# Optimization experiments

Hardware: AMD Instinct MI355X
Metric: run time of the kernel (lower is better)

The kernel has to match this reference:

```python
import jax, jax.numpy as jnp
import numpy as np

HIDDEN = 512
HEADS = 8
NORM = 1.0 / np.sqrt(HIDDEN // HEADS)  # torch: 1/sqrt(tensor(dim_k)//head) = 1/8


def setup_inputs() -> dict:
    key = jax.random.key(0)
    ks = jax.random.split(key, 14)
    B, N, D = 2, 2048, HIDDEN
    s = 0.02
    d = {
        "x_re": jax.random.normal(ks[0], (B, N, D), dtype=jnp.float32),
        "x_im": jax.random.normal(ks[1], (B, N, D), dtype=jnp.float32),
    }
    names = ["Wq_re", "Wq_im", "bq_re", "bq_im",
             "Wk_re", "Wk_im", "bk_re", "bk_im",
             "Wv_re", "Wv_im", "bv_re", "bv_im"]
    for i, nm in enumerate(names):
        shape = (D, D) if nm.startswith("W") else (D,)
        d[nm] = jax.random.normal(ks[2 + i], shape, dtype=jnp.float32) * s
    return d


def reference(x_re, x_im,
              Wq_re, Wq_im, bq_re, bq_im,
              Wk_re, Wk_im, bk_re, bk_im,
              Wv_re, Wv_im, bv_re, bv_im):
    B, N, D = x_re.shape
    h, dk = HEADS, D // HEADS
    x = jax.lax.complex(x_re, x_im)
    Wq = jax.lax.complex(Wq_re, Wq_im); bq = jax.lax.complex(bq_re, bq_im)
    Wk = jax.lax.complex(Wk_re, Wk_im); bk = jax.lax.complex(bk_re, bk_im)
    Wv = jax.lax.complex(Wv_re, Wv_im); bv = jax.lax.complex(bv_re, bv_im)

    def proj(W, b):  # torch nn.Linear: x @ W.T + b, then split heads -> [B,h,N,dk]
        y = x @ W.T + b
        return y.reshape(B, N, h, dk).transpose(0, 2, 1, 3)

    q, k, v = proj(Wq, bq), proj(Wk, bk), proj(Wv, bv)
    # complex matmul (no conjugation, matching torch.matmul), scaled
    dist = jnp.einsum("bhnd,bhmd->bhnm", q, k) * NORM
    probs = jax.nn.softmax(jnp.abs(dist), axis=-1).astype(jnp.complex64)
    att = jnp.einsum("bhnm,bhmd->bhnd", probs, v)
    att = att.transpose(0, 2, 1, 3).reshape(B, N, D)
    # real-view output [B, N, D, 2]
    return jnp.stack([att.real, att.imag], axis=-1)
```

## Files before the change

kernel.cpp:

```cpp
#include <hip/hip_runtime.h>
#include <hip/hip_bf16.h>
#include <math.h>

#define B_ 2
#define N_ 2048
#define D_ 512
#define H_ 8
#define DK_ 64
#define M_ (B_ * N_)

typedef short s16x8 __attribute__((ext_vector_type(8)));
typedef short s16x4 __attribute__((ext_vector_type(4)));
typedef float fx4   __attribute__((ext_vector_type(4)));
typedef int   ix4   __attribute__((ext_vector_type(4)));

static __device__ __forceinline__ short f2bf(float f) {
    __hip_bfloat16 h = __float2bfloat16(f);
    return __builtin_bit_cast(short, h);
}
static __device__ __forceinline__ float bf2f(short s) {
    unsigned int u = ((unsigned int)(unsigned short)s) << 16;
    return __builtin_bit_cast(float, u);
}
static __device__ __forceinline__ float fexp2(float x) {
#if __has_builtin(__builtin_amdgcn_exp2f)
    return __builtin_amdgcn_exp2f(x);
#else
    return exp2f(x);
#endif
}
static __device__ __forceinline__ float fsqrt_(float x) {
#if __has_builtin(__builtin_amdgcn_sqrtf)
    return __builtin_amdgcn_sqrtf(x);
#else
    return sqrtf(x);
#endif
}
static __device__ __forceinline__ int pack_tr(float a, float b) {
    unsigned ua = __builtin_bit_cast(unsigned, a);
    unsigned ub = __builtin_bit_cast(unsigned, b);
    return (int)((ua >> 16) | (ub & 0xFFFF0000u));
}

#define MFMA16(a, b, c) __builtin_amdgcn_mfma_f32_16x16x32_bf16(a, b, c, 0, 0, 0)

#define C2_ 0.18033688f
#define M0_ 16.0f

__global__ __launch_bounds__(256, 2)
void qkproj_mfma(const float* __restrict__ xr, const float* __restrict__ xi,
                 const float* __restrict__ W0r, const float* __restrict__ W0i,
                 const float* __restrict__ b0r, const float* __restrict__ b0i,
                 const float* __restrict__ W1r, const float* __restrict__ W1i,
                 const float* __restrict__ b1r, const float* __restrict__ b1i,
                 short* __restrict__ o0r, short* __restrict__ o0i,
                 short* __restrict__ o1r, short* __restrict__ o1i)
{
    __shared__ short sA[2][128][40];
    __shared__ short sB[2][64][40];

    const int tid = threadIdx.x;
    const int w = tid >> 6, l = tid & 63, lg = l >> 4, lc = l & 15;
    const int wr = w >> 1, wc = w & 1;
    const int bn = blockIdx.x, bm = blockIdx.y, z = blockIdx.z;
    const float* Wr = z ? W1r : W0r;
    const float* Wi = z ? W1i : W0i;
    const float* br = z ? b1r : b0r;
    const float* bi = z ? b1i : b0i;
    short* outr = z ? o1r : o0r;
    short* outi = z ? o1i : o0i;

    const int srow = tid >> 3, scol = (tid & 7) * 4;
    int aoff = (bm * 128 + srow) * D_ + scol;
    int boff = (bn * 64 + srow) * D_ + scol;

    float4 rA[8], rB[4];
    auto issue = [&]() {
#pragma unroll
        for (int u = 0; u < 8; ++u) {
            const float* src = (u >= 4) ? xi : xr;
            rA[u] = *(const float4*)&src[aoff + (u & 3) * 32 * D_];
        }
#pragma unroll
        for (int u = 0; u < 4; ++u) {
            const float* src = (u >= 2) ? Wi : Wr;
            rB[u] = *(const float4*)&src[boff + (u & 1) * 32 * D_];
        }
        aoff += 32; boff += 32;
    };

    fx4 Cre[4][2], Cim[4][2];
#pragma unroll
    for (int mf = 0; mf < 4; ++mf)
#pragma unroll
        for (int nf = 0; nf < 2; ++nf)
#pragma unroll
            for (int j = 0; j < 4; ++j) { Cre[mf][nf][j] = 0.f; Cim[mf][nf][j] = 0.f; }

    issue();
    for (int k0 = 0; k0 < D_; k0 += 32) {
        __syncthreads();
#pragma unroll
        for (int u = 0; u < 8; ++u) {
            int comp = u >> 2, row = (u & 3) * 32 + srow;
            float vv[4] = {rA[u].x, rA[u].y, rA[u].z, rA[u].w};
            s16x4 hv;
#pragma unroll
            for (int q = 0; q < 4; ++q) hv[q] = f2bf(vv[q]);
            *(s16x4*)&sA[comp][row][scol] = hv;
        }
#pragma unroll
        for (int u = 0; u < 4; ++u) {
            int comp = u >> 1, row = (u & 1) * 32 + srow;
            float vv[4] = {rB[u].x, rB[u].y, rB[u].z, rB[u].w};
            s16x4 hv;
#pragma unroll
            for (int q = 0; q < 4; ++q) hv[q] = f2bf(vv[q]);
            *(s16x4*)&sB[comp][row][scol] = hv;
        }
        __syncthreads();
        if (k0 + 32 < D_) issue();

        s16x8 a[2][4];
#pragma unroll
        for (int comp = 0; comp < 2; ++comp)
#pragma unroll
            for (int mf = 0; mf < 4; ++mf)
                a[comp][mf] = *(const s16x8*)&sA[comp][wr * 64 + mf * 16 + lc][lg * 8];
        s16x8 bfr[2][2], bin[2];
#pragma unroll
        for (int comp = 0; comp < 2; ++comp)
#pragma unroll
            for (int nf = 0; nf < 2; ++nf)
                bfr[comp][nf] = *(const s16x8*)&sB[comp][wc * 32 + nf * 16 + lc][lg * 8];
#pragma unroll
        for (int nf = 0; nf < 2; ++nf) bin[nf] = bfr[1][nf] ^ (short)0x8000;

        __builtin_amdgcn_s_setprio(1);
#pragma unroll
        for (int mf = 0; mf < 4; ++mf)
#pragma unroll
            for (int nf = 0; nf < 2; ++nf) {
                Cre[mf][nf] = MFMA16(a[0][mf], bfr[0][nf], Cre[mf][nf]);
                Cre[mf][nf] = MFMA16(a[1][mf], bin[nf],    Cre[mf][nf]);
                Cim[mf][nf] = MFMA16(a[0][mf], bfr[1][nf], Cim[mf][nf]);
                Cim[mf][nf] = MFMA16(a[1][mf], bfr[0][nf], Cim[mf][nf]);
            }
        __builtin_amdgcn_s_setprio(0);
    }

    const int bb = (bm * 128) >> 11;
#pragma unroll
    for (int nf = 0; nf < 2; ++nf) {
        const int c = bn * 64 + wc * 32 + nf * 16 + lc;
        const float brv = br[c], biv = bi[c];
        const int h = c >> 6, dd = c & 63;
        const int n00 = (bm * 128 + wr * 64 + lg * 4) & (N_ - 1);
        size_t obase = (((size_t)(bb * H_ + h) * N_) + n00) * DK_ + dd;
#pragma unroll
        for (int mf = 0; mf < 4; ++mf)
#pragma unroll
            for (int j = 0; j < 4; ++j) {
                size_t o = obase + (size_t)(mf * 16 + j) * DK_;
                outr[o] = f2bf(Cre[mf][nf][j] + brv);
                outi[o] = f2bf(Cim[mf][nf][j] + biv);
            }
    }
}

__global__ __launch_bounds__(256, 2)
void vproj_mfma(const float* __restrict__ xr, const float* __restrict__ xi,
                const float* __restrict__ Wr, const float* __restrict__ Wi,
                const float* __restrict__ br, const float* __restrict__ bi,
                short* __restrict__ outr, short* __restrict__ outi)
{
    __shared__ short sA[2][2][64][40];
    __shared__ short sB[2][2][64][40];

    const int tid = threadIdx.x;
    const int w = tid >> 6, l = tid & 63, lg = l >> 4, lc = l & 15;
    const int wr = w >> 1, wc = w & 1;
    const int bn = blockIdx.x, bm = blockIdx.y;

    const int srow = tid >> 3, scol = (tid & 7) * 4;
    int aoff = (bm * 64 + srow) * D_ + scol;
    int boff = (bn * 64 + srow) * D_ + scol;

    float4 rA[4], rB[4];
    auto issue = [&]() {
#pragma unroll
        for (int u = 0; u < 4; ++u) {
            const float* src = (u >= 2) ? xi : xr;
            rA[u] = *(const float4*)&src[aoff + (u & 1) * 32 * D_];
        }
#pragma unroll
        for (int u = 0; u < 4; ++u) {
            const float* src = (u >= 2) ? Wi : Wr;
            rB[u] = *(const float4*)&src[boff + (u & 1) * 32 * D_];
        }
        aoff += 32; boff += 32;
    };

    fx4 Cre[2][2], Cim[2][2];
#pragma unroll
    for (int mf = 0; mf < 2; ++mf)
#pragma unroll
        for (int nf = 0; nf < 2; ++nf)
#pragma unroll
            for (int j = 0; j < 4; ++j) { Cre[mf][nf][j] = 0.f; Cim[mf][nf][j] = 0.f; }

    issue();
    for (int k0 = 0; k0 < D_; k0 += 32) {
        __syncthreads();
#pragma unroll
        for (int u = 0; u < 4; ++u) {
            int comp = u >> 1, row = (u & 1) * 32 + srow;
            float vv[4] = {rA[u].x, rA[u].y, rA[u].z, rA[u].w};
            s16x4 hv, lv;
#pragma unroll
            for (int q = 0; q < 4; ++q) {
                short hh = f2bf(vv[q]);
                hv[q] = hh;
                lv[q] = f2bf(vv[q] - bf2f(hh));
            }
            *(s16x4*)&sA[comp][0][row][scol] = hv;
            *(s16x4*)&sA[comp][1][row][scol] = lv;
        }
#pragma unroll
        for (int u = 0; u < 4; ++u) {
            int comp = u >> 1, row = (u & 1) * 32 + srow;
            float vv[4] = {rB[u].x, rB[u].y, rB[u].z, rB[u].w};
            s16x4 hv, lv;
#pragma unroll
            for (int q = 0; q < 4; ++q) {
                short hh = f2bf(vv[q]);
                hv[q] = hh;
                lv[q] = f2bf(vv[q] - bf2f(hh));
            }
            *(s16x4*)&sB[comp][0][row][scol] = hv;
            *(s16x4*)&sB[comp][1][row][scol] = lv;
        }
        __syncthreads();
        if (k0 + 32 < D_) issue();

        s16x8 a[2][2][2];
#pragma unroll
        for (int comp = 0; comp < 2; ++comp)
#pragma unroll
            for (int s = 0; s < 2; ++s)
#pragma unroll
                for (int mf = 0; mf < 2; ++mf)
                    a[comp][s][mf] = *(const s16x8*)&sA[comp][s][wr * 32 + mf * 16 + lc][lg * 8];
        s16x8 bfr[2][2][2], bin[2][2];
#pragma unroll
        for (int comp = 0; comp < 2; ++comp)
#pragma unroll
            for (int s = 0; s < 2; ++s)
#pragma unroll
                for (int nf = 0; nf < 2; ++nf)
                    bfr[comp][s][nf] = *(const s16x8*)&sB[comp][s][wc * 32 + nf * 16 + lc][lg * 8];
#pragma unroll
        for (int s = 0; s < 2; ++s)
#pragma unroll
            for (int nf = 0; nf < 2; ++nf)
                bin[s][nf] = bfr[1][s][nf] ^ (short)0x8000;

        __builtin_amdgcn_s_setprio(1);
#pragma unroll
        for (int mf = 0; mf < 2; ++mf)
#pragma unroll
            for (int nf = 0; nf < 2; ++nf) {
                fx4 cr = Cre[mf][nf], ci = Cim[mf][nf];
                cr = MFMA16(a[0][0][mf], bfr[0][0][nf], cr);
                cr = MFMA16(a[1][0][mf], bin[0][nf],    cr);
                ci = MFMA16(a[0][0][mf], bfr[1][0][nf], ci);
                ci = MFMA16(a[1][0][mf], bfr[0][0][nf], ci);
                cr = MFMA16(a[0][0][mf], bfr[0][1][nf], cr);
                cr = MFMA16(a[0][1][mf], bfr[0][0][nf], cr);
                cr = MFMA16(a[1][0][mf], bin[1][nf],    cr);
                cr = MFMA16(a[1][1][mf], bin[0][nf],    cr);
                ci = MFMA16(a[0][0][mf], bfr[1][1][nf], ci);
                ci = MFMA16(a[0][1][mf], bfr[1][0][nf], ci);
                ci = MFMA16(a[1][0][mf], bfr[0][1][nf], ci);
                ci = MFMA16(a[1][1][mf], bfr[0][0][nf], ci);
                Cre[mf][nf] = cr; Cim[mf][nf] = ci;
            }
        __builtin_amdgcn_s_setprio(0);
    }

    const int bb = (bm * 64) >> 11;
#pragma unroll
    for (int nf = 0; nf < 2; ++nf) {
        const int c = bn * 64 + wc * 32 + nf * 16 + lc;
        const float brv = br[c], biv = bi[c];
        const int h = c >> 6, dd = c & 63;
#pragma unroll
        for (int mf = 0; mf < 2; ++mf) {
            int m0 = bm * 64 + wr * 32 + mf * 16 + lg * 4;
            int n0 = m0 & (N_ - 1);
            s16x4 pr, pi;
#pragma unroll
            for (int j = 0; j < 4; ++j) {
                pr[j] = f2bf(Cre[mf][nf][j] + brv);
                pi[j] = f2bf(Cim[mf][nf][j] + biv);
            }
            size_t o = (((size_t)(bb * H_ + h) * DK_) + dd) * N_ + n0;
            *(s16x4*)&outr[o] = pr;
            *(s16x4*)&outi[o] = pi;
        }
    }
}

#define NT_ (N_ / 64)

__global__ __launch_bounds__(512, 2)
void attn_mfma(const short* __restrict__ qr, const short* __restrict__ qi,
               const short* __restrict__ kr, const short* __restrict__ ki,
               const short* __restrict__ vtr, const short* __restrict__ vti,
               float* __restrict__ out)
{
    __shared__ short sK [2][64][72];
    __shared__ short sVt[2][64][72];

    const int tid = threadIdx.x;
    const int w = tid >> 6, l = tid & 63, lg = l >> 4, lc = l & 15;
    const int qt = blockIdx.x, bh = blockIdx.y;
    const int b = bh >> 3, h = bh & 7;

    s16x8 Qr[2], Qi_[2], Qin[2];
    {
        size_t base = ((size_t)bh * N_ + (size_t)qt * 128 + w * 16 + lc) * DK_ + lg * 8;
        Qr[0]  = *(const s16x8*)&qr[base];
        Qr[1]  = *(const s16x8*)&qr[base + 32];
        Qi_[0] = *(const s16x8*)&qi[base];
        Qi_[1] = *(const s16x8*)&qi[base + 32];
        Qin[0] = Qi_[0] ^ (short)0x8000;
        Qin[1] = Qi_[1] ^ (short)0x8000;
    }

    s16x8 onesf;
#pragma unroll
    for (int u = 0; u < 8; ++u) onesf[u] = (short)0x3F80;

    fx4 o_re[4], o_im[4], o_l;
#pragma unroll
    for (int dt = 0; dt < 4; ++dt)
#pragma unroll
        for (int j = 0; j < 4; ++j) { o_re[dt][j] = 0.f; o_im[dt][j] = 0.f; }
#pragma unroll
    for (int j = 0; j < 4; ++j) o_l[j] = 0.f;

    const int rS = ((lc >> 2) << 3) | (lc & 3);

    const int srow = tid >> 3, scol8 = (tid & 7) * 8;
    int koff = bh * (N_ * DK_) + srow * DK_ + scol8;
    int voff = bh * (DK_ * N_) + srow * N_ + scol8;

    s16x8 rgK[2], rgV[2];
    auto issue = [&]() {
#pragma unroll
        for (int u = 0; u < 2; ++u) {
            const short* ksrc = u ? ki : kr;
            rgK[u] = *(const s16x8*)&ksrc[koff];
            const short* vsrc = u ? vti : vtr;
            rgV[u] = *(const s16x8*)&vsrc[voff];
        }
        koff += 64 * DK_; voff += 64;
    };

    issue();
    for (int kt = 0; kt < NT_; ++kt) {
        __syncthreads();
#pragma unroll
        for (int u = 0; u < 2; ++u) {
            *(s16x8*)&sK [u][srow][scol8] = rgK[u];
            *(s16x8*)&sVt[u][srow][scol8] = rgV[u];
        }
        __syncthreads();
        if (kt + 1 < NT_) issue();

        fx4 are[4], aim[4];
#pragma unroll
        for (int t = 0; t < 4; ++t)
#pragma unroll
            for (int j = 0; j < 4; ++j) { are[t][j] = 0.f; aim[t][j] = 0.f; }

        __builtin_amdgcn_s_setprio(1);
#pragma unroll
        for (int t = 0; t < 4; ++t) {
            const int row = rS + ((t & 1) << 2) + ((t >> 1) << 5);
#pragma unroll
            for (int c = 0; c < 2; ++c) {
                s16x8 Krf = *(const s16x8*)&sK[0][row][c * 32 + lg * 8];
                s16x8 Kif = *(const s16x8*)&sK[1][row][c * 32 + lg * 8];
                are[t] = MFMA16(Krf, Qr[c],  are[t]);
                are[t] = MFMA16(Kif, Qin[c], are[t]);
                aim[t] = MFMA16(Kif, Qr[c],  aim[t]);
                aim[t] = MFMA16(Krf, Qi_[c], aim[t]);
            }
        }
        __builtin_amdgcn_s_setprio(0);

        ix4 w0, w1;
#pragma unroll
        for (int t = 0; t < 4; ++t) {
            float p[4];
#pragma unroll
            for (int j = 0; j < 4; ++j) {
                float u2 = fmaf(are[t][j], are[t][j], aim[t][j] * aim[t][j]);
                p[j] = fexp2(fmaf(C2_, fsqrt_(u2), -M0_));
            }
            int d0 = pack_tr(p[0], p[1]);
            int d1 = pack_tr(p[2], p[3]);
            if (t == 0)      { w0[0] = d0; w0[1] = d1; }
            else if (t == 1) { w0[2] = d0; w0[3] = d1; }
            else if (t == 2) { w1[0] = d0; w1[1] = d1; }
            else             { w1[2] = d0; w1[3] = d1; }
        }
        s16x8 Pf0 = __builtin_bit_cast(s16x8, w0);
        s16x8 Pf1 = __builtin_bit_cast(s16x8, w1);

        __builtin_amdgcn_s_setprio(1);
        o_l = MFMA16(Pf0, onesf, o_l);
        o_l = MFMA16(Pf1, onesf, o_l);
#pragma unroll
        for (int dt = 0; dt < 4; ++dt) {
            s16x8 Vr0 = *(const s16x8*)&sVt[0][dt * 16 + lc][lg * 8];
            s16x8 Vi0 = *(const s16x8*)&sVt[1][dt * 16 + lc][lg * 8];
            o_re[dt] = MFMA16(Pf0, Vr0, o_re[dt]);
            o_im[dt] = MFMA16(Pf0, Vi0, o_im[dt]);
            s16x8 Vr1 = *(const s16x8*)&sVt[0][dt * 16 + lc][32 + lg * 8];
            s16x8 Vi1 = *(const s16x8*)&sVt[1][dt * 16 + lc][32 + lg * 8];
            o_re[dt] = MFMA16(Pf1, Vr1, o_re[dt]);
            o_im[dt] = MFMA16(Pf1, Vi1, o_im[dt]);
        }
        __builtin_amdgcn_s_setprio(0);
    }

    float inv[4];
#pragma unroll
    for (int j = 0; j < 4; ++j) inv[j] = 1.f / o_l[j];

    float2* po = (float2*)out;
#pragma unroll
    for (int dt = 0; dt < 4; ++dt)
#pragma unroll
        for (int j = 0; j < 4; ++j) {
            int n  = qt * 128 + w * 16 + lg * 4 + j;
            int dg = h * 64 + dt * 16 + lc;
            po[((size_t)b * N_ + n) * D_ + dg] =
                make_float2(o_re[dt][j] * inv[j], o_im[dt][j] * inv[j]);
        }
}

extern "C" void kernel_launch(void* const* d_in, const int* in_sizes, int n_in,
                              void* d_out, int out_size, void* d_ws, size_t ws_size,
                              hipStream_t stream)
{
    const float* xr = (const float*)d_in[0];
    const float* xi = (const float*)d_in[1];
    const float* Wq_r = (const float*)d_in[2];
    const float* Wq_i = (const float*)d_in[3];
    const float* bq_r = (const float*)d_in[4];
    const float* bq_i = (const float*)d_in[5];
    const float* Wk_r = (const float*)d_in[6];
    const float* Wk_i = (const float*)d_in[7];
    const float* bk_r = (const float*)d_in[8];
    const float* bk_i = (const float*)d_in[9];
    const float* Wv_r = (const float*)d_in[10];
    const float* Wv_i = (const float*)d_in[11];
    const float* bv_r = (const float*)d_in[12];
    const float* bv_i = (const float*)d_in[13];

    short* ws = (short*)d_ws;
    const size_t SZ = (size_t)B_ * H_ * N_ * DK_;
    short* qr_  = ws + 0 * SZ;
    short* qi_  = ws + 1 * SZ;
    short* kr_  = ws + 2 * SZ;
    short* ki_  = ws + 3 * SZ;
    short* vtr_ = ws + 4 * SZ;
    short* vti_ = ws + 5 * SZ;

    dim3 qkgrid(D_ / 64, M_ / 128, 2);
    qkproj_mfma<<<qkgrid, 256, 0, stream>>>(xr, xi,
                                            Wq_r, Wq_i, bq_r, bq_i,
                                            Wk_r, Wk_i, bk_r, bk_i,
                                            qr_, qi_, kr_, ki_);
    dim3 vgrid(D_ / 64, M_ / 64);
    vproj_mfma<<<vgrid, 256, 0, stream>>>(xr, xi, Wv_r, Wv_i, bv_r, bv_i, vtr_, vti_);

    dim3 agrid(N_ / 128, B_ * H_);
    attn_mfma<<<agrid, 512, 0, stream>>>(qr_, qi_, kr_, ki_, vtr_, vti_, (float*)d_out);
}
```

Measured before the change: 127.3 us.

## Halve attention query tile to 64 rows and remap blocks across XCDs

The attention kernel now uses 256-thread blocks covering 64 query rows instead of 512 threads covering 128 rows, which doubles the grid to 512 blocks for better CU fill. Each thread now loads twice as many K/V fragments per tile so the 64-key staging stays the same size. Block indices are remapped so that each XCD handles two (batch, head) pairs, which keeps K/V reuse within one L2. The trade-off is that each loaded K/V tile is shared by fewer query rows, so more LDS traffic and global reads go to each unit of compute.

```diff
diff --git a/kernel.cpp b/kernel.cpp
--- a/kernel.cpp
+++ b/kernel.cpp
@@ -313,7 +313,7 @@
 
 #define NT_ (N_ / 64)
 
-__global__ __launch_bounds__(512, 2)
+__global__ __launch_bounds__(256, 2)
 void attn_mfma(const short* __restrict__ qr, const short* __restrict__ qi,
                const short* __restrict__ kr, const short* __restrict__ ki,
                const short* __restrict__ vtr, const short* __restrict__ vti,
@@ -324,12 +324,16 @@
 
     const int tid = threadIdx.x;
     const int w = tid >> 6, l = tid & 63, lg = l >> 4, lc = l & 15;
-    const int qt = blockIdx.x, bh = blockIdx.y;
+
+    const int dlin = blockIdx.y * 32 + blockIdx.x;
+    const int xcd = dlin & 7, slot = dlin >> 3;
+    const int bh = xcd * 2 + (slot >> 5);
+    const int qt = slot & 31;
     const int b = bh >> 3, h = bh & 7;
 
     s16x8 Qr[2], Qi_[2], Qin[2];
     {
-        size_t base = ((size_t)bh * N_ + (size_t)qt * 128 + w * 16 + lc) * DK_ + lg * 8;
+        size_t base = ((size_t)bh * N_ + (size_t)qt * 64 + w * 16 + lc) * DK_ + lg * 8;
         Qr[0]  = *(const s16x8*)&qr[base];
         Qr[1]  = *(const s16x8*)&qr[base + 32];
         Qi_[0] = *(const s16x8*)&qi[base];
@@ -356,26 +360,30 @@
     int koff = bh * (N_ * DK_) + srow * DK_ + scol8;
     int voff = bh * (DK_ * N_) + srow * N_ + scol8;
 
-    s16x8 rgK[2], rgV[2];
+    s16x8 rgK[4], rgV[4];
     auto issue = [&]() {
-#pragma unroll
-        for (int u = 0; u < 2; ++u) {
-            const short* ksrc = u ? ki : kr;
-            rgK[u] = *(const s16x8*)&ksrc[koff];
-            const short* vsrc = u ? vti : vtr;
-            rgV[u] = *(const s16x8*)&vsrc[voff];
-        }
+        rgK[0] = *(const s16x8*)&kr [koff];
+        rgK[1] = *(const s16x8*)&kr [koff + 32 * DK_];
+        rgK[2] = *(const s16x8*)&ki [koff];
+        rgK[3] = *(const s16x8*)&ki [koff + 32 * DK_];
+        rgV[0] = *(const s16x8*)&vtr[voff];
+        rgV[1] = *(const s16x8*)&vtr[voff + 32 * N_];
+        rgV[2] = *(const s16x8*)&vti[voff];
+        rgV[3] = *(const s16x8*)&vti[voff + 32 * N_];
         koff += 64 * DK_; voff += 64;
     };
 
     issue();
     for (int kt = 0; kt < NT_; ++kt) {
         __syncthreads();
-#pragma unroll
-        for (int u = 0; u < 2; ++u) {
-            *(s16x8*)&sK [u][srow][scol8] = rgK[u];
-            *(s16x8*)&sVt[u][srow][scol8] = rgV[u];
-        }
+        *(s16x8*)&sK [0][srow     ][scol8] = rgK[0];
+        *(s16x8*)&sK [0][srow + 32][scol8] = rgK[1];
+        *(s16x8*)&sK [1][srow     ][scol8] = rgK[2];
+        *(s16x8*)&sK [1][srow + 32][scol8] = rgK[3];
+        *(s16x8*)&sVt[0][srow     ][scol8] = rgV[0];
+        *(s16x8*)&sVt[0][srow + 32][scol8] = rgV[1];
+        *(s16x8*)&sVt[1][srow     ][scol8] = rgV[2];
+        *(s16x8*)&sVt[1][srow + 32][scol8] = rgV[3];
         __syncthreads();
         if (kt + 1 < NT_) issue();
 
@@ -446,7 +454,7 @@
     for (int dt = 0; dt < 4; ++dt)
 #pragma unroll
         for (int j = 0; j < 4; ++j) {
-            int n  = qt * 128 + w * 16 + lg * 4 + j;
+            int n  = qt * 64 + w * 16 + lg * 4 + j;
             int dg = h * 64 + dt * 16 + lc;
             po[((size_t)b * N_ + n) * D_ + dg] =
                 make_float2(o_re[dt][j] * inv[j], o_im[dt][j] * inv[j]);
@@ -489,6 +497,6 @@
     dim3 vgrid(D_ / 64, M_ / 64);
     vproj_mfma<<<vgrid, 256, 0, stream>>>(xr, xi, Wv_r, Wv_i, bv_r, bv_i, vtr_, vti_);
 
-    dim3 agrid(N_ / 128, B_ * H_);
-    attn_mfma<<<agrid, 512, 0, stream>>>(qr_, qi_, kr_, ki_, vtr_, vti_, (float*)d_out);
-}
+    dim3 agrid(N_ / 64, B_ * H_);
+    attn_mfma<<<agrid, 256, 0, stream>>>(qr_, qi_, kr_, ki_, vtr_, vti_, (float*)d_out);
+}
```

New measurement: 128.2 us. Within noise of the previous version (+0.7%).
